# Optimization experiments

Hardware: AMD Instinct MI355X
Metric: run time of the kernel (lower is better)

The kernel has to match this reference:

```python
import jax, jax.numpy as jnp
import numpy as np

B, D_IN, UNITS = 4096, 1024, 1024


def setup_inputs() -> dict:
    key = jax.random.key(0)
    ks = jax.random.split(key, 8)
    scale = 1.0 / np.sqrt(D_IN + UNITS)
    return {
        "inputs": jax.random.normal(ks[0], (B, D_IN), jnp.float32),
        "hidden_state": jax.random.normal(ks[1], (B, UNITS), jnp.float32),
        "cell_state": jax.random.normal(ks[2], (B, UNITS), jnp.float32),
        "W_f": jax.random.normal(ks[3], (D_IN + UNITS, UNITS), jnp.float32) * scale,
        "b_f": jnp.ones((UNITS,), jnp.float32),  # forget gate bias initialized to ones
        "W_i": jax.random.normal(ks[4], (D_IN + UNITS, UNITS), jnp.float32) * scale,
        "b_i": jnp.zeros((UNITS,), jnp.float32),
        "W_c": jax.random.normal(ks[5], (D_IN + UNITS, UNITS), jnp.float32) * scale,
        "b_c": jnp.zeros((UNITS,), jnp.float32),
        "W_o": jax.random.normal(ks[6], (D_IN + UNITS, UNITS), jnp.float32) * scale,
        "b_o": jnp.zeros((UNITS,), jnp.float32),
    }


def reference(inputs, hidden_state, cell_state, W_f, b_f, W_i, b_i, W_c, b_c, W_o, b_o):
    # concat (hidden, inputs) along feature axis -> [B, UNITS + D_IN]
    x = jnp.concatenate((hidden_state, inputs), axis=1)
    # fuse the 4 gate projections into one GEMM: [B, 4*UNITS]
    W = jnp.concatenate((W_f, W_i, W_c, W_o), axis=1)
    b = jnp.concatenate((b_f, b_i, b_c, b_o), axis=0)
    gates = x @ W + b
    f, i, c, o = jnp.split(gates, 4, axis=1)
    forget_gate = jax.nn.sigmoid(f)
    input_gate = jax.nn.sigmoid(i)
    state_candidates = jnp.tanh(c)
    output_gate = jax.nn.sigmoid(o)
    new_cell = forget_gate * cell_state + input_gate * state_candidates
    new_hidden = output_gate * jnp.tanh(new_cell)
    return (new_hidden, new_cell)
```

## Files before the change

kernel.cpp:

```cpp
#include <hip/hip_runtime.h>

#define MDIM 4096
#define KDIM 2048
#define UDIM 1024
#define CMOFF (MDIM * UDIM)

typedef __bf16 bfrag __attribute__((ext_vector_type(8)));
typedef float f32x4 __attribute__((ext_vector_type(4)));

#define GLDS(gsrc, ldst)                                                                  \
  __builtin_amdgcn_global_load_lds((const __attribute__((address_space(1))) void*)(gsrc), \
                                   (__attribute__((address_space(3))) void*)(ldst), 16, 0, 0)

__device__ __forceinline__ unsigned short f2bf(float x) {
  unsigned int u = __float_as_uint(x);
  unsigned int r = (u + 0x7fffu + ((u >> 16) & 1u)) >> 16;
  return (unsigned short)r;
}

__device__ __forceinline__ float fast_sigmoid(float x) {
  return 1.f / (1.f + __expf(-x));
}

__device__ __forceinline__ float fast_tanh(float x) {
  float ax = fabsf(x);
  float e = __expf(-2.f * ax);
  float r = (1.f - e) / (1.f + e);
  return copysignf(r, x);
}

__global__ void pack_x(const float* __restrict__ hidden, const float* __restrict__ inputs,
                       unsigned short* __restrict__ A) {
  int t = blockIdx.x * blockDim.x + threadIdx.x;
  int e = t * 4;
  int m = e >> 11;
  int c = e & 2047;
  const float* src = (c < 1024) ? (hidden + m * 1024 + c) : (inputs + m * 1024 + (c - 1024));
  float4 v = *(const float4*)src;
  ushort4 o;
  o.x = f2bf(v.x);
  o.y = f2bf(v.y);
  o.z = f2bf(v.z);
  o.w = f2bf(v.w);
  *(ushort4*)(A + e) = o;
}

__global__ void pack_w(const float* __restrict__ Wf, const float* __restrict__ Wi,
                       const float* __restrict__ Wc, const float* __restrict__ Wo,
                       unsigned short* __restrict__ Wt) {
  __shared__ float tile[32][33];
  const int k0 = blockIdx.x * 32;
  const int u0 = blockIdx.y * 32;
  const int g = blockIdx.z;
  const float* W = (g == 0) ? Wf : (g == 1) ? Wi : (g == 2) ? Wc : Wo;
  const int t = threadIdx.x;
  {
    int kk = t >> 3, uu = (t & 7) * 4;
    float4 v = *(const float4*)(W + (k0 + kk) * UDIM + u0 + uu);
    tile[kk][uu + 0] = v.x;
    tile[kk][uu + 1] = v.y;
    tile[kk][uu + 2] = v.z;
    tile[kk][uu + 3] = v.w;
  }
  __syncthreads();
  {
    int ur = t >> 3, k4 = (t & 7) * 4;
    ushort4 o;
    o.x = f2bf(tile[k4 + 0][ur]);
    o.y = f2bf(tile[k4 + 1][ur]);
    o.z = f2bf(tile[k4 + 2][ur]);
    o.w = f2bf(tile[k4 + 3][ur]);
    *(ushort4*)(Wt + (size_t)(g * UDIM + u0 + ur) * KDIM + k0 + k4) = o;
  }
}

__global__ __launch_bounds__(256, 2) void lstm_gemm(
    const unsigned short* __restrict__ A, const unsigned short* __restrict__ Wt,
    const float* __restrict__ bf_, const float* __restrict__ bi_,
    const float* __restrict__ bc_, const float* __restrict__ bo_,
    const float* __restrict__ cell, float* __restrict__ out) {
  __shared__ __bf16 As[128][64];
  __shared__ __bf16 Bs[128][64];

  const int m0 = blockIdx.x * 128;
  const int u0 = blockIdx.y * 32;
  const int t = threadIdx.x;
  const int lane = t & 63;
  const int w = t >> 6;
  const int lrow = lane & 15;
  const int kblk = (lane >> 4) * 8;

  f32x4 acc[2][8];
#pragma unroll
  for (int i = 0; i < 2; ++i)
#pragma unroll
    for (int j = 0; j < 8; ++j) acc[i][j] = (f32x4){0.f, 0.f, 0.f, 0.f};

  const int trow = t >> 3;
  const int tcol = (t & 7) * 8;
  const unsigned short* Ag = A + (size_t)(m0 + trow) * KDIM + tcol;
  const unsigned short* Bg = Wt + (size_t)(u0 + trow) * KDIM + tcol;
  __bf16* AsL = &As[0][0] + t * 8;
  __bf16* BsL = &Bs[0][0] + t * 8;

  for (int ks = 0; ks < KDIM; ks += 64) {
#pragma unroll
    for (int q = 0; q < 4; ++q) GLDS(Ag + (size_t)q * 32 * KDIM + ks, AsL + q * 2048);
#pragma unroll
    for (int q = 0; q < 4; ++q) GLDS(Bg + (size_t)q * UDIM * KDIM + ks, BsL + q * 2048);
    __syncthreads();
#pragma unroll
    for (int kk = 0; kk < 2; ++kk) {
      bfrag a0 = *(const bfrag*)&As[w * 32 + lrow][kk * 32 + kblk];
      bfrag a1 = *(const bfrag*)&As[w * 32 + 16 + lrow][kk * 32 + kblk];
#pragma unroll
      for (int nf = 0; nf < 8; ++nf) {
        bfrag b = *(const bfrag*)&Bs[nf * 16 + lrow][kk * 32 + kblk];
        acc[0][nf] = __builtin_amdgcn_mfma_f32_16x16x32_bf16(a0, b, acc[0][nf], 0, 0, 0);
        acc[1][nf] = __builtin_amdgcn_mfma_f32_16x16x32_bf16(a1, b, acc[1][nf], 0, 0, 0);
      }
    }
    __syncthreads();
  }

  const int rbase = m0 + w * 32 + (lane >> 4) * 4;
#pragma unroll
  for (int mi = 0; mi < 2; ++mi) {
#pragma unroll
    for (int uu = 0; uu < 2; ++uu) {
      const int u = u0 + uu * 16 + lrow;
      const float vbf = bf_[u];
      const float vbi = bi_[u];
      const float vbc = bc_[u];
      const float vbo = bo_[u];
#pragma unroll
      for (int j = 0; j < 4; ++j) {
        const int m = rbase + mi * 16 + j;
        float pf = acc[mi][0 + uu][j] + vbf;
        float pi = acc[mi][2 + uu][j] + vbi;
        float pc = acc[mi][4 + uu][j] + vbc;
        float po = acc[mi][6 + uu][j] + vbo;
        float fg = fast_sigmoid(pf);
        float ig = fast_sigmoid(pi);
        float cc = fast_tanh(pc);
        float og = fast_sigmoid(po);
        float cold = cell[m * UDIM + u];
        float cnew = fg * cold + ig * cc;
        float hnew = og * fast_tanh(cnew);
        out[m * UDIM + u] = hnew;
        out[CMOFF + m * UDIM + u] = cnew;
      }
    }
  }
}

extern "C" void kernel_launch(void* const* d_in, const int* in_sizes, int n_in,
                              void* d_out, int out_size, void* d_ws, size_t ws_size,
                              hipStream_t stream) {
  const float* inputs = (const float*)d_in[0];
  const float* hidden = (const float*)d_in[1];
  const float* cell = (const float*)d_in[2];
  const float* Wf = (const float*)d_in[3];
  const float* bf = (const float*)d_in[4];
  const float* Wi = (const float*)d_in[5];
  const float* bi = (const float*)d_in[6];
  const float* Wc = (const float*)d_in[7];
  const float* bc = (const float*)d_in[8];
  const float* Wo = (const float*)d_in[9];
  const float* bo = (const float*)d_in[10];
  float* out = (float*)d_out;

  unsigned short* Abf = (unsigned short*)d_ws;
  unsigned short* Wt = Abf + (size_t)MDIM * KDIM;

  pack_x<<<(MDIM * KDIM / 4) / 256, 256, 0, stream>>>(hidden, inputs, Abf);
  pack_w<<<dim3(KDIM / 32, UDIM / 32, 4), 256, 0, stream>>>(Wf, Wi, Wc, Wo, Wt);
  lstm_gemm<<<dim3(MDIM / 128, UDIM / 32), 256, 0, stream>>>(Abf, Wt, bf, bi, bc, bo, cell, out);
}
```

Before: 111.7 us.

## Rewrite LSTM GEMM with 256x256 tiles, 4-stage LDS pipeline and swizzle

Replaces the 128x128 (M x 4-gate) block tile with a 256x256 tile computed by 8 waves, using a 4-deep ring of LDS buffers with K-step 32 and async global-to-LDS loads issued three tiles ahead. LDS addresses are XOR-swizzled to avoid bank conflicts, and the workgroup order is remapped for L2 locality. The loop interleaves MFMA bursts with barriers, explicit vmcnt waits and setprio. This aims to cut global reload traffic and memory stalls. In exchange it needs 128KB of dynamic LDS per block, which limits occupancy, and it adds many barriers per K step.

```diff
diff --git a/kernel.cpp b/kernel.cpp
--- a/kernel.cpp
+++ b/kernel.cpp
@@ -4,6 +4,8 @@
 #define KDIM 2048
 #define UDIM 1024
 #define CMOFF (MDIM * UDIM)
+#define NK 64
+#define THREADS 512
 
 typedef __bf16 bfrag __attribute__((ext_vector_type(8)));
 typedef float f32x4 __attribute__((ext_vector_type(4)));
@@ -18,9 +20,7 @@
   return (unsigned short)r;
 }
 
-__device__ __forceinline__ float fast_sigmoid(float x) {
-  return 1.f / (1.f + __expf(-x));
-}
+__device__ __forceinline__ float fast_sigmoid(float x) { return 1.f / (1.f + __expf(-x)); }
 
 __device__ __forceinline__ float fast_tanh(float x) {
   float ax = fabsf(x);
@@ -74,82 +74,150 @@
   }
 }
 
-__global__ __launch_bounds__(256, 2) void lstm_gemm(
+__global__ __launch_bounds__(THREADS, 2) void lstm_gemm(
     const unsigned short* __restrict__ A, const unsigned short* __restrict__ Wt,
     const float* __restrict__ bf_, const float* __restrict__ bi_,
     const float* __restrict__ bc_, const float* __restrict__ bo_,
     const float* __restrict__ cell, float* __restrict__ out) {
-  __shared__ __bf16 As[128][64];
-  __shared__ __bf16 Bs[128][64];
-
-  const int m0 = blockIdx.x * 128;
-  const int u0 = blockIdx.y * 32;
-  const int t = threadIdx.x;
-  const int lane = t & 63;
-  const int w = t >> 6;
+  extern __shared__ __bf16 lds[];
+
+  const int tid = threadIdx.x;
+  const int lane = tid & 63;
+  const int wid = tid >> 6;
+  const int wr = wid >> 2;
+  const int wc = wid & 3;
   const int lrow = lane & 15;
-  const int kblk = (lane >> 4) * 8;
-
-  f32x4 acc[2][8];
-#pragma unroll
-  for (int i = 0; i < 2; ++i)
-#pragma unroll
-    for (int j = 0; j < 8; ++j) acc[i][j] = (f32x4){0.f, 0.f, 0.f, 0.f};
-
-  const int trow = t >> 3;
-  const int tcol = (t & 7) * 8;
-  const unsigned short* Ag = A + (size_t)(m0 + trow) * KDIM + tcol;
-  const unsigned short* Bg = Wt + (size_t)(u0 + trow) * KDIM + tcol;
-  __bf16* AsL = &As[0][0] + t * 8;
-  __bf16* BsL = &Bs[0][0] + t * 8;
-
-  for (int ks = 0; ks < KDIM; ks += 64) {
-#pragma unroll
-    for (int q = 0; q < 4; ++q) GLDS(Ag + (size_t)q * 32 * KDIM + ks, AsL + q * 2048);
-#pragma unroll
-    for (int q = 0; q < 4; ++q) GLDS(Bg + (size_t)q * UDIM * KDIM + ks, BsL + q * 2048);
-    __syncthreads();
-#pragma unroll
-    for (int kk = 0; kk < 2; ++kk) {
-      bfrag a0 = *(const bfrag*)&As[w * 32 + lrow][kk * 32 + kblk];
-      bfrag a1 = *(const bfrag*)&As[w * 32 + 16 + lrow][kk * 32 + kblk];
-#pragma unroll
-      for (int nf = 0; nf < 8; ++nf) {
-        bfrag b = *(const bfrag*)&Bs[nf * 16 + lrow][kk * 32 + kblk];
-        acc[0][nf] = __builtin_amdgcn_mfma_f32_16x16x32_bf16(a0, b, acc[0][nf], 0, 0, 0);
-        acc[1][nf] = __builtin_amdgcn_mfma_f32_16x16x32_bf16(a1, b, acc[1][nf], 0, 0, 0);
-      }
-    }
-    __syncthreads();
-  }
-
-  const int rbase = m0 + w * 32 + (lane >> 4) * 4;
-#pragma unroll
-  for (int mi = 0; mi < 2; ++mi) {
-#pragma unroll
-    for (int uu = 0; uu < 2; ++uu) {
-      const int u = u0 + uu * 16 + lrow;
-      const float vbf = bf_[u];
-      const float vbi = bi_[u];
-      const float vbc = bc_[u];
-      const float vbo = bo_[u];
-#pragma unroll
-      for (int j = 0; j < 4; ++j) {
-        const int m = rbase + mi * 16 + j;
-        float pf = acc[mi][0 + uu][j] + vbf;
-        float pi = acc[mi][2 + uu][j] + vbi;
-        float pc = acc[mi][4 + uu][j] + vbc;
-        float po = acc[mi][6 + uu][j] + vbo;
-        float fg = fast_sigmoid(pf);
-        float ig = fast_sigmoid(pi);
-        float cc = fast_tanh(pc);
-        float og = fast_sigmoid(po);
-        float cold = cell[m * UDIM + u];
-        float cnew = fg * cold + ig * cc;
-        float hnew = og * fast_tanh(cnew);
-        out[m * UDIM + u] = hnew;
-        out[CMOFF + m * UDIM + u] = cnew;
-      }
+  const int gb = lane >> 4;
+
+  const int wg = blockIdx.x;
+  const int swz = (wg & 7) * 32 + (wg >> 3);
+  const int m0 = (swz >> 4) * 256;
+  const int bn = swz & 15;
+
+  const int G0 = tid, G1 = THREADS + tid;
+  const int ar0 = G0 >> 2, ar1 = G1 >> 2;
+  const unsigned short* aS0 =
+      A + (size_t)(m0 + ar0) * KDIM + (((G0 & 3) ^ ((ar0 >> 1) & 3)) * 8);
+  const unsigned short* aS1 =
+      A + (size_t)(m0 + ar1) * KDIM + (((G1 & 3) ^ ((ar1 >> 1) & 3)) * 8);
+  const int nr0 = G0 >> 2, nr1 = G1 >> 2;
+  const int u_0 = bn * 64 + ((nr0 >> 6) << 4) + (nr0 & 15);
+  const int u_1 = bn * 64 + ((nr1 >> 6) << 4) + (nr1 & 15);
+  const int g_0 = (nr0 >> 4) & 3;
+  const int g_1 = (nr1 >> 4) & 3;
+  const unsigned short* bS0 =
+      Wt + (size_t)(g_0 * UDIM + u_0) * KDIM + (((G0 & 3) ^ ((nr0 >> 1) & 3)) * 8);
+  const unsigned short* bS1 =
+      Wt + (size_t)(g_1 * UDIM + u_1) * KDIM + (((G1 & 3) ^ ((nr1 >> 1) & 3)) * 8);
+
+  int aoff[8];
+#pragma unroll
+  for (int mi = 0; mi < 8; ++mi) {
+    const int R = wr * 128 + mi * 16 + lrow;
+    aoff[mi] = R * 32 + ((gb ^ ((R >> 1) & 3)) * 8);
+  }
+  int boff[4];
+#pragma unroll
+  for (int nf = 0; nf < 4; ++nf) {
+    const int n = wc * 64 + nf * 16 + lrow;
+    boff[nf] = 8192 + n * 32 + ((gb ^ ((n >> 1) & 3)) * 8);
+  }
+
+  f32x4 acc[8][4];
+#pragma unroll
+  for (int mi = 0; mi < 8; ++mi)
+#pragma unroll
+    for (int nf = 0; nf < 4; ++nf) acc[mi][nf] = (f32x4){0.f, 0.f, 0.f, 0.f};
+
+#define STAGE_A(T)                                     \
+  do {                                                 \
+    __bf16* dst_ = lds + ((T) & 3) * 16384;            \
+    GLDS(aS0 + (T) * 32, dst_ + G0 * 8);               \
+    GLDS(aS1 + (T) * 32, dst_ + G1 * 8);               \
+  } while (0)
+#define STAGE_B(T)                                     \
+  do {                                                 \
+    __bf16* dst_ = lds + ((T) & 3) * 16384 + 8192;     \
+    GLDS(bS0 + (T) * 32, dst_ + G0 * 8);               \
+    GLDS(bS1 + (T) * 32, dst_ + G1 * 8);               \
+  } while (0)
+
+  STAGE_A(0);
+  STAGE_B(0);
+  STAGE_A(1);
+  STAGE_B(1);
+  STAGE_A(2);
+  STAGE_B(2);
+  __builtin_amdgcn_sched_barrier(0);
+  asm volatile("s_waitcnt vmcnt(8)" ::: "memory");
+  __builtin_amdgcn_s_barrier();
+  __builtin_amdgcn_sched_barrier(0);
+
+#define TILE_BODY(T, DO_STAGE, WAITCODE)                                                       \
+  do {                                                                                         \
+    __bf16* ldsr_ = lds + ((T) & 3) * 16384;                                                   \
+    bfrag Af[8];                                                                               \
+    _Pragma("unroll") for (int mi = 0; mi < 8; ++mi) Af[mi] = *(const bfrag*)(ldsr_ + aoff[mi]); \
+    bfrag Bf0 = *(const bfrag*)(ldsr_ + boff[0]);                                              \
+    bfrag Bf1 = *(const bfrag*)(ldsr_ + boff[1]);                                              \
+    if (DO_STAGE) STAGE_A((T) + 3);                                                            \
+    __builtin_amdgcn_sched_barrier(0);                                                         \
+    __builtin_amdgcn_s_barrier();                                                              \
+    __builtin_amdgcn_sched_barrier(0);                                                         \
+    __builtin_amdgcn_s_setprio(1);                                                             \
+    _Pragma("unroll") for (int mi = 0; mi < 8; ++mi) acc[mi][0] =                              \
+        __builtin_amdgcn_mfma_f32_16x16x32_bf16(Af[mi], Bf0, acc[mi][0], 0, 0, 0);             \
+    _Pragma("unroll") for (int mi = 0; mi < 8; ++mi) acc[mi][1] =                              \
+        __builtin_amdgcn_mfma_f32_16x16x32_bf16(Af[mi], Bf1, acc[mi][1], 0, 0, 0);             \
+    __builtin_amdgcn_s_setprio(0);                                                             \
+    __builtin_amdgcn_sched_barrier(0);                                                         \
+    __builtin_amdgcn_s_barrier();                                                              \
+    __builtin_amdgcn_sched_barrier(0);                                                         \
+    bfrag Bf2 = *(const bfrag*)(ldsr_ + boff[2]);                                              \
+    bfrag Bf3 = *(const bfrag*)(ldsr_ + boff[3]);                                              \
+    if (DO_STAGE) STAGE_B((T) + 3);                                                            \
+    __builtin_amdgcn_sched_barrier(0);                                                         \
+    __builtin_amdgcn_s_barrier();                                                              \
+    __builtin_amdgcn_sched_barrier(0);                                                         \
+    __builtin_amdgcn_s_setprio(1);                                                             \
+    _Pragma("unroll") for (int mi = 0; mi < 8; ++mi) acc[mi][2] =                              \
+        __builtin_amdgcn_mfma_f32_16x16x32_bf16(Af[mi], Bf2, acc[mi][2], 0, 0, 0);             \
+    _Pragma("unroll") for (int mi = 0; mi < 8; ++mi) acc[mi][3] =                              \
+        __builtin_amdgcn_mfma_f32_16x16x32_bf16(Af[mi], Bf3, acc[mi][3], 0, 0, 0);             \
+    __builtin_amdgcn_s_setprio(0);                                                             \
+    __builtin_amdgcn_sched_barrier(0);                                                         \
+    WAITCODE;                                                                                  \
+    __builtin_amdgcn_s_barrier();                                                              \
+    __builtin_amdgcn_sched_barrier(0);                                                         \
+  } while (0)
+
+  for (int t = 0; t <= NK - 4; ++t) {
+    TILE_BODY(t, 1, asm volatile("s_waitcnt vmcnt(8)" ::: "memory"));
+  }
+  TILE_BODY(NK - 3, 0, asm volatile("s_waitcnt vmcnt(4)" ::: "memory"));
+  TILE_BODY(NK - 2, 0, asm volatile("s_waitcnt vmcnt(0)" ::: "memory"));
+  TILE_BODY(NK - 1, 0, );
+
+  const int u = bn * 64 + wc * 16 + lrow;
+  const float fb = bf_[u], ib = bi_[u], cb = bc_[u], ob = bo_[u];
+  const int rbase = m0 + wr * 128 + (lane >> 4) * 4;
+#pragma unroll
+  for (int mi = 0; mi < 8; ++mi) {
+#pragma unroll
+    for (int j = 0; j < 4; ++j) {
+      const int m = rbase + mi * 16 + j;
+      float pf = acc[mi][0][j] + fb;
+      float pi = acc[mi][1][j] + ib;
+      float pc = acc[mi][2][j] + cb;
+      float po = acc[mi][3][j] + ob;
+      float fg = fast_sigmoid(pf);
+      float ig = fast_sigmoid(pi);
+      float cc = fast_tanh(pc);
+      float og = fast_sigmoid(po);
+      float cold = cell[(size_t)m * UDIM + u];
+      float cnew = fg * cold + ig * cc;
+      out[(size_t)m * UDIM + u] = og * fast_tanh(cnew);
+      out[CMOFF + (size_t)m * UDIM + u] = cnew;
     }
   }
 }
@@ -175,5 +243,5 @@
 
   pack_x<<<(MDIM * KDIM / 4) / 256, 256, 0, stream>>>(hidden, inputs, Abf);
   pack_w<<<dim3(KDIM / 32, UDIM / 32, 4), 256, 0, stream>>>(Wf, Wi, Wc, Wo, Wt);
-  lstm_gemm<<<dim3(MDIM / 128, UDIM / 32), 256, 0, stream>>>(Abf, Wt, bf, bi, bc, bo, cell, out);
-}
+  lstm_gemm<<<dim3(256), dim3(THREADS), 131072, stream>>>(Abf, Wt, bf, bi, bc, bo, cell, out);
+}
```

Result: faster. 92.34 us (-17.3%).
